# Performance work log

Hardware: AMD Instinct MI355X
Metric: run time of the kernel (lower is better)

Reference implementation:

```python
import jax, jax.numpy as jnp
import numpy as np

B, S, D, H = 2, 2048, 1024, 16
HD = D // H  # head_dim = 64


def setup_inputs() -> dict:
    key = jax.random.key(0)
    ks = jax.random.split(key, 10)
    std = 1.0 / np.sqrt(D)
    inputs = jax.random.normal(ks[0], (B, S, D), dtype=jnp.float32)
    # stacked per-head projection weights: [H, HD, D] (row-major like nn.Linear)
    Wq = jax.random.uniform(ks[1], (H, HD, D), jnp.float32, -std, std)
    bq = jax.random.uniform(ks[2], (H, HD), jnp.float32, -std, std)
    Wk = jax.random.uniform(ks[3], (H, HD, D), jnp.float32, -std, std)
    bk = jax.random.uniform(ks[4], (H, HD), jnp.float32, -std, std)
    Wv = jax.random.uniform(ks[5], (H, HD, D), jnp.float32, -std, std)
    bv = jax.random.uniform(ks[6], (H, HD), jnp.float32, -std, std)
    Wo = jax.random.uniform(ks[7], (D, D), jnp.float32, -std, std)
    bo = jax.random.uniform(ks[8], (D,), jnp.float32, -std, std)
    return {"inputs": inputs, "Wq": Wq, "bq": bq, "Wk": Wk, "bk": bk,
            "Wv": Wv, "bv": bv, "Wo": Wo, "bo": bo}


def reference(inputs, Wq, bq, Wk, bk, Wv, bv, Wo, bo):
    # per-head projections, batched over heads: [B,H,S,HD]
    q = jnp.einsum('bsd,hed->bhse', inputs, Wq) + bq[None, :, None, :]
    k = jnp.einsum('bsd,hed->bhse', inputs, Wk) + bk[None, :, None, :]
    v = jnp.einsum('bsd,hed->bhse', inputs, Wv) + bv[None, :, None, :]
    scale = 1.0 / np.sqrt(HD).astype(np.float32)
    # explicit [B,H,S,S] score matrix, as in the original naive attention
    scores = jnp.einsum('bhqe,bhke->bhqk', q, k) * scale
    causal = jnp.tril(jnp.ones((S, S), dtype=bool))
    scores = jnp.where(causal[None, None], scores, jnp.float32(-jnp.inf))
    attn = jax.nn.softmax(scores, axis=-1)  # dropout p=0 -> identity
    wv = jnp.einsum('bhqk,bhke->bhqe', attn, v)
    # concat heads along feature dim: [B,S,H*HD] = [B,S,D]
    z = wv.transpose(0, 2, 1, 3).reshape(B, S, D)
    out = jnp.einsum('bsd,ed->bse', z, Wo) + bo
    return out
```

## Files before the change

### kernel.cpp

```cpp
#include <hip/hip_runtime.h>
#include <math.h>

#define Bx 2
#define Sx 2048
#define Dx 1024
#define Hx 16
#define HDx 64
#define Mx (Bx*Sx)

typedef __bf16 bf16x8 __attribute__((ext_vector_type(8)));
typedef __bf16 bf16x4 __attribute__((ext_vector_type(4)));
typedef float  f32x4  __attribute__((ext_vector_type(4)));

#define SCL 0.18033688011112042f

__device__ __forceinline__ void gload_lds16(const __bf16* g, __bf16* l) {
  __builtin_amdgcn_global_load_lds(
      (const __attribute__((address_space(1))) unsigned int*)g,
      (__attribute__((address_space(3))) unsigned int*)l, 16, 0, 0);
}

__device__ __forceinline__ void cvt8(const float* s, __bf16* d) {
  float4 a = *(const float4*)s;
  float4 b = *(const float4*)(s + 4);
  bf16x8 o;
  o[0] = (__bf16)a.x; o[1] = (__bf16)a.y; o[2] = (__bf16)a.z; o[3] = (__bf16)a.w;
  o[4] = (__bf16)b.x; o[5] = (__bf16)b.y; o[6] = (__bf16)b.z; o[7] = (__bf16)b.w;
  *(bf16x8*)d = o;
}

__global__ __launch_bounds__(256) void cvt_kernel(
    const float* __restrict__ x, const float* __restrict__ Wq,
    const float* __restrict__ Wk, const float* __restrict__ Wv,
    const float* __restrict__ Wo, const float* __restrict__ bq,
    const float* __restrict__ bk, const float* __restrict__ bv,
    __bf16* __restrict__ xb, __bf16* __restrict__ wqkv,
    __bf16* __restrict__ wob, float* __restrict__ bqkv)
{
  const int bid = blockIdx.x;
  const int t = threadIdx.x;
  const size_t MEG = 1024u * 1024u;
  if (bid < 2048) {
    size_t e = (size_t)bid * 2048 + t * 8;
    cvt8(x + e, xb + e);
  } else if (bid < 3584) {
    size_t e = (size_t)(bid - 2048) * 2048 + t * 8;
    const float* src = (e < MEG) ? (Wq + e) : (e < 2 * MEG) ? (Wk + (e - MEG)) : (Wv + (e - 2 * MEG));
    cvt8(src, wqkv + e);
  } else if (bid < 4096) {
    size_t e = (size_t)(bid - 3584) * 2048 + t * 8;
    cvt8(Wo + e, wob + e);
  } else {
    for (int i = t; i < 3072; i += 256)
      bqkv[i] = (i < 1024) ? bq[i] : (i < 2048) ? bk[i - 1024] : bv[i - 2048];
  }
}

template<int TM, int TN, int MODE>
__global__ __launch_bounds__(256) void gemm_k(
    const __bf16* __restrict__ A, const __bf16* __restrict__ W,
    const float* __restrict__ bias, float* __restrict__ Cf,
    __bf16* __restrict__ Cb, __bf16* __restrict__ vT,
    int M, int N, int K, int ldc)
{
  constexpr int MS = TM / 32;
  constexpr int NS = TN / 32;
  __shared__ __bf16 As[TM * 32];
  __shared__ __bf16 Bs[TN * 32];
  const int tid = threadIdx.x;
  const int lane = tid & 63, wave = tid >> 6;
  const int l16 = lane & 15, quad = lane >> 4;
  const int wm = (wave >> 1) * (TM / 2);
  const int wn = (wave & 1) * (TN / 2);
  const int m0 = blockIdx.y * TM;
  const int n0 = blockIdx.x * TN;

  const f32x4 zero = {0.f, 0.f, 0.f, 0.f};
  f32x4 acc[MS][NS];
#pragma unroll
  for (int i = 0; i < MS; ++i)
#pragma unroll
    for (int j = 0; j < NS; ++j) acc[i][j] = zero;

  const int arow = tid >> 2;
  const int achk = (tid & 3) * 8;
  const __bf16* Ag = A + (size_t)(m0 + arow) * K + achk;
  const __bf16* Wg = W + (size_t)(n0 + arow) * K + achk;

  for (int k0 = 0; k0 < K; k0 += 32) {
    __syncthreads();
#pragma unroll
    for (int i = 0; i < TM / 64; ++i)
      gload_lds16(Ag + (size_t)i * 64 * K + k0, &As[(i * 256 + tid) * 8]);
#pragma unroll
    for (int i = 0; i < TN / 64; ++i)
      gload_lds16(Wg + (size_t)i * 64 * K + k0, &Bs[(i * 256 + tid) * 8]);
    __syncthreads();

    bf16x8 af[MS], bfr[NS];
#pragma unroll
    for (int i = 0; i < MS; ++i)
      af[i] = *(const bf16x8*)&As[(wm + i * 16 + l16) * 32 + quad * 8];
#pragma unroll
    for (int j = 0; j < NS; ++j)
      bfr[j] = *(const bf16x8*)&Bs[(wn + j * 16 + l16) * 32 + quad * 8];
#pragma unroll
    for (int i = 0; i < MS; ++i)
#pragma unroll
      for (int j = 0; j < NS; ++j)
        acc[i][j] = __builtin_amdgcn_mfma_f32_16x16x32_bf16(af[i], bfr[j], acc[i][j], 0, 0, 0);
  }

  const int cbase = n0 + wn + l16;
#pragma unroll
  for (int j = 0; j < NS; ++j) {
    const int c = cbase + j * 16;
    const float bv_ = bias[c];
#pragma unroll
    for (int i = 0; i < MS; ++i) {
      const int r0 = m0 + wm + i * 16 + quad * 4;
      if (MODE == 0) {
#pragma unroll
        for (int g = 0; g < 4; ++g)
          Cf[(size_t)(r0 + g) * ldc + c] = acc[i][j][g] + bv_;
      } else {
        if (c < 2048) {
          const float sc = (c < 1024) ? SCL : 1.0f;
#pragma unroll
          for (int g = 0; g < 4; ++g)
            Cb[(size_t)(r0 + g) * 3072 + c] = (__bf16)((acc[i][j][g] + bv_) * sc);
        } else {
          const int c2 = c - 2048;
          const int hh = c2 >> 6, dd = c2 & 63;
          const int bb = r0 >> 11, ss = r0 & 2047;
          bf16x4 st;
          st[0] = (__bf16)(acc[i][j][0] + bv_);
          st[1] = (__bf16)(acc[i][j][1] + bv_);
          st[2] = (__bf16)(acc[i][j][2] + bv_);
          st[3] = (__bf16)(acc[i][j][3] + bv_);
          *(bf16x4*)&vT[((size_t)(bb * 16 + hh) * 64 + dd) * 2048 + ss] = st;
        }
      }
    }
  }
}

__global__ __launch_bounds__(256) void attn_mfma(
    const __bf16* __restrict__ qkv, const __bf16* __restrict__ vT,
    __bf16* __restrict__ zb)
{
  __shared__ __bf16 Qs[64 * 64];
  __shared__ __bf16 Ks[2][64 * 64];
  __shared__ __bf16 Vs[2][64 * 64];
  __shared__ __bf16 Ps[4][16 * 64];

  const int tid = threadIdx.x;
  const int lane = tid & 63, wave = tid >> 6;
  const int l16 = lane & 15, quad = lane >> 4;
  const int bx = blockIdx.x;
  const int qt = 31 - (bx >> 5);
  const int bh = bx & 31;
  const int h = bh & 15, b = bh >> 4;
  const int q0 = qt * 64;

  const __bf16* qg = qkv + (size_t)b * 2048 * 3072 + h * 64;
  const __bf16* kg = qg + 1024;
  const __bf16* vg = vT + (size_t)bh * 64 * 2048;

  const int srow = tid >> 3;
  (void)srow;

#pragma unroll
  for (int i = 0; i < 2; ++i) {
    int slot = i * 256 + tid;
    int row = slot >> 3, ph = slot & 7;
    int cs = ph ^ (row & 7);
    gload_lds16(qg + (size_t)(q0 + row) * 3072 + cs * 8, &Qs[slot * 8]);
    gload_lds16(kg + (size_t)row * 3072 + cs * 8, &Ks[0][slot * 8]);
    gload_lds16(vg + (size_t)row * 2048 + cs * 8, &Vs[0][slot * 8]);
  }
  __syncthreads();

  const int sw0 = ((quad) ^ (l16 & 7)) * 8;
  const int sw1 = ((quad + 4) ^ (l16 & 7)) * 8;
  const int mrow = wave * 16 + l16;

  bf16x8 qf0 = *(const bf16x8*)&Qs[mrow * 64 + sw0];
  bf16x8 qf1 = *(const bf16x8*)&Qs[mrow * 64 + sw1];

  const f32x4 zero = {0.f, 0.f, 0.f, 0.f};
  f32x4 O[4];
  float lp[4] = {0.f, 0.f, 0.f, 0.f};
#pragma unroll
  for (int j = 0; j < 4; ++j) O[j] = zero;

  const int rq = q0 + wave * 16 + quad * 4;
  __bf16* P = Ps[wave];

  for (int kt = 0; kt <= qt; ++kt) {
    const int bb = kt & 1;
    if (kt < qt) {
      const int kn = (kt + 1) * 64;
      const int nb = bb ^ 1;
#pragma unroll
      for (int i = 0; i < 2; ++i) {
        int slot = i * 256 + tid;
        int row = slot >> 3, ph = slot & 7;
        int cs = ph ^ (row & 7);
        gload_lds16(kg + (size_t)(kn + row) * 3072 + cs * 8, &Ks[nb][slot * 8]);
        gload_lds16(vg + (size_t)row * 2048 + kn + cs * 8, &Vs[nb][slot * 8]);
      }
    }

    f32x4 s_[4];
#pragma unroll
    for (int j = 0; j < 4; ++j) s_[j] = zero;
#pragma unroll
    for (int j = 0; j < 4; ++j) {
      bf16x8 kf0 = *(const bf16x8*)&Ks[bb][(j * 16 + l16) * 64 + sw0];
      s_[j] = __builtin_amdgcn_mfma_f32_16x16x32_bf16(qf0, kf0, s_[j], 0, 0, 0);
      bf16x8 kf1 = *(const bf16x8*)&Ks[bb][(j * 16 + l16) * 64 + sw1];
      s_[j] = __builtin_amdgcn_mfma_f32_16x16x32_bf16(qf1, kf1, s_[j], 0, 0, 0);
    }

    const int k0 = kt * 64;
    const bool dg = (kt == qt);
#pragma unroll
    for (int j = 0; j < 4; ++j) {
      const int cg = k0 + j * 16 + l16;
#pragma unroll
      for (int g = 0; g < 4; ++g) {
        float p = __builtin_exp2f(s_[j][g]);
        if (dg && cg > rq + g) p = 0.f;
        s_[j][g] = p;
        lp[g] += p;
      }
    }

#pragma unroll
    for (int j = 0; j < 4; ++j) {
      const int col = j * 16 + l16;
      const int ch = col >> 3, cin = col & 7;
#pragma unroll
      for (int g = 0; g < 4; ++g) {
        const int row = quad * 4 + g;
        P[row * 64 + ((ch ^ (row & 7)) * 8) + cin] = (__bf16)s_[j][g];
      }
    }

    {
      bf16x8 pf0 = *(const bf16x8*)&P[l16 * 64 + sw0];
      bf16x8 pf1 = *(const bf16x8*)&P[l16 * 64 + sw1];
#pragma unroll
      for (int j = 0; j < 4; ++j) {
        bf16x8 vf0 = *(const bf16x8*)&Vs[bb][(j * 16 + l16) * 64 + sw0];
        O[j] = __builtin_amdgcn_mfma_f32_16x16x32_bf16(pf0, vf0, O[j], 0, 0, 0);
        bf16x8 vf1 = *(const bf16x8*)&Vs[bb][(j * 16 + l16) * 64 + sw1];
        O[j] = __builtin_amdgcn_mfma_f32_16x16x32_bf16(pf1, vf1, O[j], 0, 0, 0);
      }
    }

    if (kt < qt) __syncthreads();
  }

  float inv[4];
#pragma unroll
  for (int g = 0; g < 4; ++g) {
    float s = lp[g];
#pragma unroll
    for (int d = 1; d < 16; d <<= 1) s += __shfl_xor(s, d);
    inv[g] = 1.0f / s;
  }
#pragma unroll
  for (int g = 0; g < 4; ++g) {
    const size_t rb = (size_t)(b * 2048 + rq + g) * 1024 + h * 64 + l16;
#pragma unroll
    for (int j = 0; j < 4; ++j)
      zb[rb + j * 16] = (__bf16)(O[j][g] * inv[g]);
  }
}

extern "C" void kernel_launch(void* const* d_in, const int* in_sizes, int n_in,
                              void* d_out, int out_size, void* d_ws, size_t ws_size,
                              hipStream_t stream) {
  (void)in_sizes; (void)n_in; (void)out_size; (void)ws_size;
  const float* x  = (const float*)d_in[0];
  const float* Wq = (const float*)d_in[1];
  const float* bq = (const float*)d_in[2];
  const float* Wk = (const float*)d_in[3];
  const float* bk = (const float*)d_in[4];
  const float* Wv = (const float*)d_in[5];
  const float* bv = (const float*)d_in[6];
  const float* Wo = (const float*)d_in[7];
  const float* bo = (const float*)d_in[8];

  char* ws = (char*)d_ws;
  __bf16* xb   = (__bf16*)(ws);
  __bf16* wqkv = (__bf16*)(ws + (8ull  << 20));
  __bf16* wob  = (__bf16*)(ws + (14ull << 20));
  float*  bqkv = (float*) (ws + (16ull << 20));
  __bf16* qkv  = (__bf16*)(ws + (17ull << 20));
  __bf16* vT   = (__bf16*)(ws + (41ull << 20));
  __bf16* zb   = (__bf16*)(ws + (49ull << 20));

  cvt_kernel<<<4097, 256, 0, stream>>>(x, Wq, Wk, Wv, Wo, bq, bk, bv,
                                       xb, wqkv, wob, bqkv);
  gemm_k<128, 128, 1><<<dim3(24, 32), 256, 0, stream>>>(
      xb, wqkv, bqkv, nullptr, qkv, vT, Mx, 3072, 1024, 0);
  attn_mfma<<<1024, 256, 0, stream>>>(qkv, vT, zb);
  gemm_k<128, 128, 0><<<dim3(8, 32), 256, 0, stream>>>(
      zb, wob, bo, (float*)d_out, nullptr, nullptr, Mx, 1024, 1024, 1024);
}
```

Measured before the change: 199.4 us.

## Peel diagonal attention tile, compute row sums via MFMA, reuse Q LDS for P

The attention loop is split into unmasked off-diagonal tiles and one peeled diagonal tile, so the causal mask check leaves the main loop. Softmax row sums are now taken with an extra MFMA against a ones vector instead of per-element adds plus a shuffle reduction. The P staging buffer reuses the Q shared-memory region, which lowers LDS use and may raise occupancy. The output projection GEMM also switches to 128x64 tiles with twice as many blocks, trading per-block reuse for more parallelism.

After: 198.3 us. Within noise of the previous version (-0.5%).

```diff
diff --git a/kernel.cpp b/kernel.cpp
--- a/kernel.cpp
+++ b/kernel.cpp
@@ -152,7 +152,6 @@
   __shared__ __bf16 Qs[64 * 64];
   __shared__ __bf16 Ks[2][64 * 64];
   __shared__ __bf16 Vs[2][64 * 64];
-  __shared__ __bf16 Ps[4][16 * 64];
 
   const int tid = threadIdx.x;
   const int lane = tid & 63, wave = tid >> 6;
@@ -167,9 +166,6 @@
   const __bf16* kg = qg + 1024;
   const __bf16* vg = vT + (size_t)bh * 64 * 2048;
 
-  const int srow = tid >> 3;
-  (void)srow;
-
 #pragma unroll
   for (int i = 0; i < 2; ++i) {
     int slot = i * 256 + tid;
@@ -187,96 +183,93 @@
 
   bf16x8 qf0 = *(const bf16x8*)&Qs[mrow * 64 + sw0];
   bf16x8 qf1 = *(const bf16x8*)&Qs[mrow * 64 + sw1];
+  __bf16* P = &Qs[wave * 16 * 64];
+
+  bf16x8 onesf;
+  {
+    __bf16 ov = (l16 == 0) ? (__bf16)1.0f : (__bf16)0.0f;
+#pragma unroll
+    for (int i = 0; i < 8; ++i) onesf[i] = ov;
+  }
 
   const f32x4 zero = {0.f, 0.f, 0.f, 0.f};
-  f32x4 O[4];
-  float lp[4] = {0.f, 0.f, 0.f, 0.f};
+  f32x4 O[4], Ol = zero;
 #pragma unroll
   for (int j = 0; j < 4; ++j) O[j] = zero;
 
   const int rq = q0 + wave * 16 + quad * 4;
-  __bf16* P = Ps[wave];
-
-  for (int kt = 0; kt <= qt; ++kt) {
+
+#define ATTN_TILE(bb, DIAG)                                                     \
+  {                                                                             \
+    f32x4 s_[4];                                                                \
+    _Pragma("unroll")                                                           \
+    for (int j = 0; j < 4; ++j) s_[j] = zero;                                   \
+    _Pragma("unroll")                                                           \
+    for (int j = 0; j < 4; ++j) {                                               \
+      bf16x8 kf0 = *(const bf16x8*)&Ks[bb][(j * 16 + l16) * 64 + sw0];          \
+      s_[j] = __builtin_amdgcn_mfma_f32_16x16x32_bf16(qf0, kf0, s_[j], 0, 0, 0);\
+      bf16x8 kf1 = *(const bf16x8*)&Ks[bb][(j * 16 + l16) * 64 + sw1];          \
+      s_[j] = __builtin_amdgcn_mfma_f32_16x16x32_bf16(qf1, kf1, s_[j], 0, 0, 0);\
+    }                                                                           \
+    _Pragma("unroll")                                                           \
+    for (int j = 0; j < 4; ++j) {                                               \
+      _Pragma("unroll")                                                         \
+      for (int g = 0; g < 4; ++g) {                                             \
+        float p = __builtin_exp2f(s_[j][g]);                                    \
+        if (DIAG && (j * 16 + l16) > (wave * 16 + quad * 4 + g)) p = 0.f;       \
+        s_[j][g] = p;                                                           \
+      }                                                                         \
+    }                                                                           \
+    _Pragma("unroll")                                                           \
+    for (int j = 0; j < 4; ++j) {                                               \
+      const int col = j * 16 + l16;                                             \
+      const int ch = col >> 3, cin = col & 7;                                   \
+      _Pragma("unroll")                                                         \
+      for (int g = 0; g < 4; ++g) {                                             \
+        const int row = quad * 4 + g;                                           \
+        P[row * 64 + ((ch ^ (row & 7)) * 8) + cin] = (__bf16)s_[j][g];          \
+      }                                                                         \
+    }                                                                           \
+    {                                                                           \
+      bf16x8 pf0 = *(const bf16x8*)&P[l16 * 64 + sw0];                          \
+      bf16x8 pf1 = *(const bf16x8*)&P[l16 * 64 + sw1];                          \
+      _Pragma("unroll")                                                         \
+      for (int j = 0; j < 4; ++j) {                                             \
+        bf16x8 vf0 = *(const bf16x8*)&Vs[bb][(j * 16 + l16) * 64 + sw0];        \
+        O[j] = __builtin_amdgcn_mfma_f32_16x16x32_bf16(pf0, vf0, O[j], 0, 0, 0);\
+        bf16x8 vf1 = *(const bf16x8*)&Vs[bb][(j * 16 + l16) * 64 + sw1];        \
+        O[j] = __builtin_amdgcn_mfma_f32_16x16x32_bf16(pf1, vf1, O[j], 0, 0, 0);\
+      }                                                                         \
+      Ol = __builtin_amdgcn_mfma_f32_16x16x32_bf16(pf0, onesf, Ol, 0, 0, 0);    \
+      Ol = __builtin_amdgcn_mfma_f32_16x16x32_bf16(pf1, onesf, Ol, 0, 0, 0);    \
+    }                                                                           \
+  }
+
+  for (int kt = 0; kt < qt; ++kt) {
     const int bb = kt & 1;
-    if (kt < qt) {
-      const int kn = (kt + 1) * 64;
-      const int nb = bb ^ 1;
-#pragma unroll
-      for (int i = 0; i < 2; ++i) {
-        int slot = i * 256 + tid;
-        int row = slot >> 3, ph = slot & 7;
-        int cs = ph ^ (row & 7);
-        gload_lds16(kg + (size_t)(kn + row) * 3072 + cs * 8, &Ks[nb][slot * 8]);
-        gload_lds16(vg + (size_t)row * 2048 + kn + cs * 8, &Vs[nb][slot * 8]);
-      }
+    const int kn = (kt + 1) * 64;
+    const int nb = bb ^ 1;
+#pragma unroll
+    for (int i = 0; i < 2; ++i) {
+      int slot = i * 256 + tid;
+      int row = slot >> 3, ph = slot & 7;
+      int cs = ph ^ (row & 7);
+      gload_lds16(kg + (size_t)(kn + row) * 3072 + cs * 8, &Ks[nb][slot * 8]);
+      gload_lds16(vg + (size_t)row * 2048 + kn + cs * 8, &Vs[nb][slot * 8]);
     }
-
-    f32x4 s_[4];
-#pragma unroll
-    for (int j = 0; j < 4; ++j) s_[j] = zero;
-#pragma unroll
-    for (int j = 0; j < 4; ++j) {
-      bf16x8 kf0 = *(const bf16x8*)&Ks[bb][(j * 16 + l16) * 64 + sw0];
-      s_[j] = __builtin_amdgcn_mfma_f32_16x16x32_bf16(qf0, kf0, s_[j], 0, 0, 0);
-      bf16x8 kf1 = *(const bf16x8*)&Ks[bb][(j * 16 + l16) * 64 + sw1];
-      s_[j] = __builtin_amdgcn_mfma_f32_16x16x32_bf16(qf1, kf1, s_[j], 0, 0, 0);
-    }
-
-    const int k0 = kt * 64;
-    const bool dg = (kt == qt);
-#pragma unroll
-    for (int j = 0; j < 4; ++j) {
-      const int cg = k0 + j * 16 + l16;
-#pragma unroll
-      for (int g = 0; g < 4; ++g) {
-        float p = __builtin_exp2f(s_[j][g]);
-        if (dg && cg > rq + g) p = 0.f;
-        s_[j][g] = p;
-        lp[g] += p;
-      }
-    }
-
-#pragma unroll
-    for (int j = 0; j < 4; ++j) {
-      const int col = j * 16 + l16;
-      const int ch = col >> 3, cin = col & 7;
-#pragma unroll
-      for (int g = 0; g < 4; ++g) {
-        const int row = quad * 4 + g;
-        P[row * 64 + ((ch ^ (row & 7)) * 8) + cin] = (__bf16)s_[j][g];
-      }
-    }
-
-    {
-      bf16x8 pf0 = *(const bf16x8*)&P[l16 * 64 + sw0];
-      bf16x8 pf1 = *(const bf16x8*)&P[l16 * 64 + sw1];
-#pragma unroll
-      for (int j = 0; j < 4; ++j) {
-        bf16x8 vf0 = *(const bf16x8*)&Vs[bb][(j * 16 + l16) * 64 + sw0];
-        O[j] = __builtin_amdgcn_mfma_f32_16x16x32_bf16(pf0, vf0, O[j], 0, 0, 0);
-        bf16x8 vf1 = *(const bf16x8*)&Vs[bb][(j * 16 + l16) * 64 + sw1];
-        O[j] = __builtin_amdgcn_mfma_f32_16x16x32_bf16(pf1, vf1, O[j], 0, 0, 0);
-      }
-    }
-
-    if (kt < qt) __syncthreads();
-  }
-
-  float inv[4];
+    ATTN_TILE(bb, false)
+    __syncthreads();
+  }
+  ATTN_TILE((qt & 1), true)
+
 #pragma unroll
   for (int g = 0; g < 4; ++g) {
-    float s = lp[g];
-#pragma unroll
-    for (int d = 1; d < 16; d <<= 1) s += __shfl_xor(s, d);
-    inv[g] = 1.0f / s;
-  }
-#pragma unroll
-  for (int g = 0; g < 4; ++g) {
+    const float lv = __shfl(Ol[g], lane & 48);
+    const float inv = 1.0f / lv;
     const size_t rb = (size_t)(b * 2048 + rq + g) * 1024 + h * 64 + l16;
 #pragma unroll
     for (int j = 0; j < 4; ++j)
-      zb[rb + j * 16] = (__bf16)(O[j][g] * inv[g]);
+      zb[rb + j * 16] = (__bf16)(O[j][g] * inv);
   }
 }
 
@@ -308,6 +301,6 @@
   gemm_k<128, 128, 1><<<dim3(24, 32), 256, 0, stream>>>(
       xb, wqkv, bqkv, nullptr, qkv, vT, Mx, 3072, 1024, 0);
   attn_mfma<<<1024, 256, 0, stream>>>(qkv, vT, zb);
-  gemm_k<128, 128, 0><<<dim3(8, 32), 256, 0, stream>>>(
+  gemm_k<128, 64, 0><<<dim3(16, 32), 256, 0, stream>>>(
       zb, wob, bo, (float*)d_out, nullptr, nullptr, Mx, 1024, 1024, 1024);
 }
```
